# Kernel tuning notes

Measured on AMD Instinct MI355X. Metric: run time of the kernel, lower is better.

Reference implementation:

```python
import jax, jax.numpy as jnp
import numpy as np

B, BANDS, N, IN_C, F, C = 4096, 5, 30, 512, 128, 9

def setup_inputs() -> dict:
    key = jax.random.key(0)
    ks = jax.random.split(key, 10)
    def glorot(k, shape):
        lim = float(np.sqrt(6.0 / (shape[0] + shape[-1])))
        return jax.random.uniform(k, shape, jnp.float32, -lim, lim)
    return {
        "real": jax.random.normal(ks[0], (B, N, IN_C), jnp.float32),
        "imag": jax.random.normal(ks[1], (B, N, IN_C), jnp.float32),
        "graph": jax.random.normal(ks[2], (B, BANDS, N, N), jnp.float32),
        "W1": glorot(ks[3], (IN_C, F)),
        "b1": jnp.zeros((F,), jnp.float32),
        "W2": glorot(ks[4], (F, F)),
        "b2": jnp.zeros((F,), jnp.float32),
        "Wlin": glorot(ks[5], (F, 1)),
        "blin": jnp.zeros((1,), jnp.float32),
        "Wconv": glorot(ks[6], (C, N)),  # Conv1d(30, C, k=1) weight squeezed
        "bconv": jnp.zeros((C,), jnp.float32),
    }

def _norm_adj(graph):
    # adj = mean over bands; PyG from_scipy_sparse_matrix keeps only the
    # nonzero PATTERN (edge weights are discarded in the original code).
    adj = jnp.mean(graph, axis=1)                       # [B, N, N]
    A = (adj != 0).astype(jnp.float32)
    eye = jnp.eye(A.shape[-1], dtype=jnp.float32)
    A_hat = jnp.where(eye > 0, 1.0, A)                  # add remaining self-loops
    deg = A_hat.sum(-1)                                 # [B, N]
    dinv = jnp.where(deg > 0, jax.lax.rsqrt(deg), 0.0)
    return dinv[..., :, None] * A_hat * dinv[..., None, :]  # D^-1/2 (A+I) D^-1/2

def reference(real, imag, graph, W1, b1, W2, b2, Wlin, blin, Wconv, bconv):
    An = _norm_adj(graph)                               # [B, N, N]
    # GCNConv layer 1: propagate(x @ W) + bias, then ReLU (dropout = eval identity)
    h = jnp.einsum('bnm,bmf->bnf', An, real @ W1) + b1
    h = jax.nn.relu(h)
    # GCNConv layer 2
    h = jnp.einsum('bnm,bmf->bnf', An, h @ W2) + b2
    h = jax.nn.relu(h)
    # lin: [B, N, F] -> [B, N], relu, then Conv1d(30->C, k=1) over length-1 axis
    x = jax.nn.relu((h @ Wlin + blin).squeeze(-1))      # [B, N]
    out = x @ Wconv.T + bconv                           # [B, C]
    return out
```

## Files before the change

kernel.cpp:

```cpp
#include <hip/hip_runtime.h>
#include <cstdint>

#define B_SZ 4096
#define NN   30
#define INC  512
#define FF   128
#define CC   9

typedef short short8 __attribute__((ext_vector_type(8)));
typedef float f32x4 __attribute__((ext_vector_type(4)));
typedef unsigned short us4 __attribute__((ext_vector_type(4)));

__device__ inline void split_bf16(float x, unsigned short& hi, unsigned short& lo) {
  uint32_t bits = __float_as_uint(x);
  hi = (unsigned short)(bits >> 16);
  float hif = __uint_as_float(((uint32_t)hi) << 16);
  float r = x - hif;
  lo = (unsigned short)(__float_as_uint(r) >> 16);
}

__global__ __launch_bounds__(128) void k_norm_adj(const float* __restrict__ graph,
                                                  float* __restrict__ An) {
  __shared__ float Ah[NN * NN];
  __shared__ float dinv[NN];
  const int b = blockIdx.x;
  const float* g = graph + (long)b * 5 * NN * NN;
  for (int e = threadIdx.x; e < NN * NN; e += 128) {
    float s = g[e] + g[e + 900] + g[e + 1800] + g[e + 2700] + g[e + 3600];
    float mean = s * 0.2f;
    int i = e / NN;
    int j = e - i * NN;
    Ah[e] = (mean != 0.0f || i == j) ? 1.0f : 0.0f;
  }
  __syncthreads();
  if (threadIdx.x < NN) {
    float d = 0.f;
#pragma unroll
    for (int j = 0; j < NN; ++j) d += Ah[threadIdx.x * NN + j];
    dinv[threadIdx.x] = (d > 0.f) ? (1.0f / sqrtf(d)) : 0.0f;
  }
  __syncthreads();
  float* ob = An + (long)b * NN * NN;
  for (int e = threadIdx.x; e < NN * NN; e += 128) {
    int i = e / NN;
    int j = e - i * NN;
    ob[e] = Ah[e] * dinv[i] * dinv[j];
  }
}

__global__ __launch_bounds__(256) void k_prep_w(const float* __restrict__ W,
                                                unsigned short* __restrict__ Wth,
                                                unsigned short* __restrict__ Wtl,
                                                int K) {
  int idx = blockIdx.x * 256 + threadIdx.x;
  if (idx >= K * FF) return;
  int k = idx >> 7;
  int n = idx & 127;
  unsigned short h, l;
  split_bf16(W[idx], h, l);
  Wth[n * K + k] = h;
  Wtl[n * K + k] = l;
}

template <int K>
__global__ __launch_bounds__(256) void k_gemm_mfma(const float* __restrict__ A,
                                                   const unsigned short* __restrict__ Bth,
                                                   const unsigned short* __restrict__ Btl,
                                                   float* __restrict__ C) {
  constexpr int BK = 32;
  constexpr int LDT = 48;
  __shared__ unsigned short Ash[128 * LDT];
  __shared__ unsigned short Asl[128 * LDT];
  __shared__ unsigned short Bsh[128 * LDT];
  __shared__ unsigned short Bsl[128 * LDT];

  const int tid = threadIdx.x;
  const int wave = tid >> 6;
  const int lane = tid & 63;
  const int wrow = (wave >> 1) * 64;
  const int wcol = (wave & 1) * 64;
  const int fr = lane & 15;
  const int fq = lane >> 4;
  const long m0 = (long)blockIdx.x * 128;

  f32x4 acc[4][4];
#pragma unroll
  for (int i = 0; i < 4; ++i)
#pragma unroll
    for (int j = 0; j < 4; ++j) acc[i][j] = (f32x4){0.f, 0.f, 0.f, 0.f};

  for (int k0 = 0; k0 < K; k0 += BK) {
#pragma unroll
    for (int it = 0; it < 4; ++it) {
      int f = tid + it * 256;
      int row = f >> 3;
      int kq = f & 7;
      float4 v = *(const float4*)(A + (m0 + row) * (long)K + k0 + kq * 4);
      us4 h, l;
      split_bf16(v.x, ((unsigned short*)&h)[0], ((unsigned short*)&l)[0]);
      split_bf16(v.y, ((unsigned short*)&h)[1], ((unsigned short*)&l)[1]);
      split_bf16(v.z, ((unsigned short*)&h)[2], ((unsigned short*)&l)[2]);
      split_bf16(v.w, ((unsigned short*)&h)[3], ((unsigned short*)&l)[3]);
      *(us4*)(Ash + row * LDT + kq * 4) = h;
      *(us4*)(Asl + row * LDT + kq * 4) = l;
    }
#pragma unroll
    for (int it = 0; it < 4; ++it) {
      int f = tid + it * 256;
      int n = f >> 3;
      int kq = f & 7;
      us4 vh = *(const us4*)(Bth + (long)n * K + k0 + kq * 4);
      us4 vl = *(const us4*)(Btl + (long)n * K + k0 + kq * 4);
      *(us4*)(Bsh + n * LDT + kq * 4) = vh;
      *(us4*)(Bsl + n * LDT + kq * 4) = vl;
    }
    __syncthreads();

    short8 bh[4], bl[4];
#pragma unroll
    for (int ct = 0; ct < 4; ++ct) {
      int n = wcol + ct * 16 + fr;
      bh[ct] = *(const short8*)(Bsh + n * LDT + fq * 8);
      bl[ct] = *(const short8*)(Bsl + n * LDT + fq * 8);
    }
#pragma unroll
    for (int rt = 0; rt < 4; ++rt) {
      int m = wrow + rt * 16 + fr;
      short8 ah = *(const short8*)(Ash + m * LDT + fq * 8);
      short8 al = *(const short8*)(Asl + m * LDT + fq * 8);
#pragma unroll
      for (int ct = 0; ct < 4; ++ct) {
        acc[rt][ct] = __builtin_amdgcn_mfma_f32_16x16x32_bf16(ah, bh[ct], acc[rt][ct], 0, 0, 0);
        acc[rt][ct] = __builtin_amdgcn_mfma_f32_16x16x32_bf16(al, bh[ct], acc[rt][ct], 0, 0, 0);
        acc[rt][ct] = __builtin_amdgcn_mfma_f32_16x16x32_bf16(ah, bl[ct], acc[rt][ct], 0, 0, 0);
      }
    }
    __syncthreads();
  }

#pragma unroll
  for (int rt = 0; rt < 4; ++rt) {
#pragma unroll
    for (int ct = 0; ct < 4; ++ct) {
      int col = wcol + ct * 16 + fr;
#pragma unroll
      for (int r = 0; r < 4; ++r) {
        long row = m0 + wrow + rt * 16 + fq * 4 + r;
        C[row * FF + col] = acc[rt][ct][r];
      }
    }
  }
}

__global__ __launch_bounds__(128) void k_prop1(const float* __restrict__ An,
                                               const float* __restrict__ Y,
                                               const float* __restrict__ b1,
                                               float* __restrict__ H1) {
  const int b = blockIdx.x;
  const int f = threadIdx.x;
  const float* Yb = Y + (long)b * NN * FF + f;
  float y[NN];
#pragma unroll
  for (int m = 0; m < NN; ++m) y[m] = Yb[m * FF];
  const float* Ab = An + (long)b * NN * NN;
  const float bias = b1[f];
  float* Hb = H1 + (long)b * NN * FF + f;
#pragma unroll 1
  for (int i = 0; i < NN; ++i) {
    float acc = bias;
#pragma unroll
    for (int m = 0; m < NN; ++m) acc = fmaf(Ab[i * NN + m], y[m], acc);
    Hb[i * FF] = fmaxf(acc, 0.f);
  }
}

__global__ __launch_bounds__(128) void k_final(const float* __restrict__ An,
                                               const float* __restrict__ T,
                                               const float* __restrict__ b2,
                                               const float* __restrict__ Wlin,
                                               const float* __restrict__ blin,
                                               const float* __restrict__ Wconv,
                                               const float* __restrict__ bconv,
                                               float* __restrict__ out) {
  __shared__ float partial[2][NN];
  __shared__ float xs[NN];
  const int b = blockIdx.x;
  const int f = threadIdx.x;
  const int wave = f >> 6;
  const int lane = f & 63;
  const float* Tb = T + (long)b * NN * FF + f;
  float t[NN];
#pragma unroll
  for (int m = 0; m < NN; ++m) t[m] = Tb[m * FF];
  const float* Ab = An + (long)b * NN * NN;
  const float bias = b2[f];
  const float wl = Wlin[f];
#pragma unroll 1
  for (int i = 0; i < NN; ++i) {
    float acc = bias;
#pragma unroll
    for (int m = 0; m < NN; ++m) acc = fmaf(Ab[i * NN + m], t[m], acc);
    float c = fmaxf(acc, 0.f) * wl;
#pragma unroll
    for (int off = 32; off > 0; off >>= 1) c += __shfl_down(c, off, 64);
    if (lane == 0) partial[wave][i] = c;
  }
  __syncthreads();
  if (f < NN) {
    float x = partial[0][f] + partial[1][f] + blin[0];
    xs[f] = fmaxf(x, 0.f);
  }
  __syncthreads();
  if (f < CC) {
    float o = bconv[f];
#pragma unroll
    for (int i = 0; i < NN; ++i) o = fmaf(xs[i], Wconv[f * NN + i], o);
    out[(long)b * CC + f] = o;
  }
}

extern "C" void kernel_launch(void* const* d_in, const int* in_sizes, int n_in,
                              void* d_out, int out_size, void* d_ws, size_t ws_size,
                              hipStream_t stream) {
  const float* real  = (const float*)d_in[0];
  const float* graph = (const float*)d_in[2];
  const float* W1    = (const float*)d_in[3];
  const float* b1    = (const float*)d_in[4];
  const float* W2    = (const float*)d_in[5];
  const float* b2    = (const float*)d_in[6];
  const float* Wlin  = (const float*)d_in[7];
  const float* blin  = (const float*)d_in[8];
  const float* Wconv = (const float*)d_in[9];
  const float* bconv = (const float*)d_in[10];
  float* out = (float*)d_out;

  float* An = (float*)d_ws;
  float* Y  = An + (long)B_SZ * NN * NN;
  float* H1 = Y + (long)B_SZ * NN * FF;
  unsigned short* W1th = (unsigned short*)(H1 + (long)B_SZ * NN * FF);
  unsigned short* W1tl = W1th + INC * FF;
  unsigned short* W2th = W1tl + INC * FF;
  unsigned short* W2tl = W2th + FF * FF;
  float* T = Y;

  const int M = B_SZ * NN;

  k_norm_adj<<<B_SZ, 128, 0, stream>>>(graph, An);
  k_prep_w<<<(INC * FF + 255) / 256, 256, 0, stream>>>(W1, W1th, W1tl, INC);
  k_prep_w<<<(FF * FF + 255) / 256, 256, 0, stream>>>(W2, W2th, W2tl, FF);
  k_gemm_mfma<INC><<<M / 128, 256, 0, stream>>>(real, W1th, W1tl, Y);
  k_prop1<<<B_SZ, 128, 0, stream>>>(An, Y, b1, H1);
  k_gemm_mfma<FF><<<M / 128, 256, 0, stream>>>(H1, W2th, W2tl, T);
  k_final<<<B_SZ, 128, 0, stream>>>(An, T, b2, Wlin, blin, Wconv, bconv, out);
}
```

Baseline: 632.9 us.

## Fuse both GEMMs and propagations into one per-graph-pair kernel

Replaces the two MFMA GEMM kernels and the two propagation kernels with one kernel that processes two graphs per block (64 padded rows). Intermediate Y, H1 and T stay in LDS, with an XOR swizzle on H1 to avoid bank conflicts, so the large global round-trips of the intermediates are removed. The A tile is register-prefetched one K-step ahead, while W1/W2 fragments are read straight from global (L2). The trade-off is padding 60 rows to 64, the occupancy cap from about 64KB of LDS per block, and weight reloads from L2 in every block.

```diff
diff --git a/kernel.cpp b/kernel.cpp
--- a/kernel.cpp
+++ b/kernel.cpp
@@ -62,160 +62,216 @@
   Wtl[n * K + k] = l;
 }
 
-template <int K>
-__global__ __launch_bounds__(256) void k_gemm_mfma(const float* __restrict__ A,
-                                                   const unsigned short* __restrict__ Bth,
-                                                   const unsigned short* __restrict__ Btl,
-                                                   float* __restrict__ C) {
-  constexpr int BK = 32;
-  constexpr int LDT = 48;
-  __shared__ unsigned short Ash[128 * LDT];
-  __shared__ unsigned short Asl[128 * LDT];
-  __shared__ unsigned short Bsh[128 * LDT];
-  __shared__ unsigned short Bsl[128 * LDT];
+#define LDT 40
+#define LDY 132
+
+__global__ __launch_bounds__(256, 2) void k_fused(
+    const float* __restrict__ real,
+    const float* __restrict__ An,
+    const unsigned short* __restrict__ W1h, const unsigned short* __restrict__ W1l,
+    const unsigned short* __restrict__ W2h, const unsigned short* __restrict__ W2l,
+    const float* __restrict__ b1v, const float* __restrict__ b2v,
+    const float* __restrict__ Wlin, const float* __restrict__ blin,
+    const float* __restrict__ Wconv, const float* __restrict__ bconv,
+    float* __restrict__ out) {
+  __shared__ __align__(16) char smem[65168];
+  unsigned short* H1h = (unsigned short*)smem;
+  unsigned short* H1l = (unsigned short*)(smem + 16384);
+  unsigned short* Ash = (unsigned short*)(smem + 32768);
+  unsigned short* Asl = (unsigned short*)(smem + 32768 + 64 * LDT * 2);
+  float* Ylds = (float*)(smem + 32768);
+  float* partial = (float*)(smem + 64448);
+  float* xs = (float*)(smem + 64928);
 
   const int tid = threadIdx.x;
   const int wave = tid >> 6;
   const int lane = tid & 63;
-  const int wrow = (wave >> 1) * 64;
-  const int wcol = (wave & 1) * 64;
   const int fr = lane & 15;
   const int fq = lane >> 4;
-  const long m0 = (long)blockIdx.x * 128;
-
-  f32x4 acc[4][4];
+  const int wc = wave;
+  const long b0 = (long)blockIdx.x * 2;
+
+  f32x4 acc[4][2];
 #pragma unroll
   for (int i = 0; i < 4; ++i)
 #pragma unroll
-    for (int j = 0; j < 4; ++j) acc[i][j] = (f32x4){0.f, 0.f, 0.f, 0.f};
-
-  for (int k0 = 0; k0 < K; k0 += BK) {
-#pragma unroll
-    for (int it = 0; it < 4; ++it) {
-      int f = tid + it * 256;
-      int row = f >> 3;
-      int kq = f & 7;
-      float4 v = *(const float4*)(A + (m0 + row) * (long)K + k0 + kq * 4);
+    for (int j = 0; j < 2; ++j) acc[i][j] = (f32x4){0.f, 0.f, 0.f, 0.f};
+
+  const int r0 = tid >> 3, kq0 = tid & 7;
+  const int r1 = r0 + 32;
+  int i0 = r0 & 31; if (i0 >= NN) i0 -= NN;
+  int i1 = r1 & 31; if (i1 >= NN) i1 -= NN;
+  const float* aptr0 = real + ((b0 + (r0 >> 5)) * NN + i0) * (long)INC + kq0 * 4;
+  const float* aptr1 = real + ((b0 + (r1 >> 5)) * NN + i1) * (long)INC + kq0 * 4;
+
+  float4 pA0 = *(const float4*)(aptr0);
+  float4 pA1 = *(const float4*)(aptr1);
+
+  for (int k0 = 0; k0 < INC; k0 += 32) {
+    __syncthreads();
+    {
       us4 h, l;
-      split_bf16(v.x, ((unsigned short*)&h)[0], ((unsigned short*)&l)[0]);
-      split_bf16(v.y, ((unsigned short*)&h)[1], ((unsigned short*)&l)[1]);
-      split_bf16(v.z, ((unsigned short*)&h)[2], ((unsigned short*)&l)[2]);
-      split_bf16(v.w, ((unsigned short*)&h)[3], ((unsigned short*)&l)[3]);
-      *(us4*)(Ash + row * LDT + kq * 4) = h;
-      *(us4*)(Asl + row * LDT + kq * 4) = l;
-    }
-#pragma unroll
-    for (int it = 0; it < 4; ++it) {
-      int f = tid + it * 256;
-      int n = f >> 3;
-      int kq = f & 7;
-      us4 vh = *(const us4*)(Bth + (long)n * K + k0 + kq * 4);
-      us4 vl = *(const us4*)(Btl + (long)n * K + k0 + kq * 4);
-      *(us4*)(Bsh + n * LDT + kq * 4) = vh;
-      *(us4*)(Bsl + n * LDT + kq * 4) = vl;
+      split_bf16(pA0.x, ((unsigned short*)&h)[0], ((unsigned short*)&l)[0]);
+      split_bf16(pA0.y, ((unsigned short*)&h)[1], ((unsigned short*)&l)[1]);
+      split_bf16(pA0.z, ((unsigned short*)&h)[2], ((unsigned short*)&l)[2]);
+      split_bf16(pA0.w, ((unsigned short*)&h)[3], ((unsigned short*)&l)[3]);
+      *(us4*)(Ash + r0 * LDT + kq0 * 4) = h;
+      *(us4*)(Asl + r0 * LDT + kq0 * 4) = l;
+      split_bf16(pA1.x, ((unsigned short*)&h)[0], ((unsigned short*)&l)[0]);
+      split_bf16(pA1.y, ((unsigned short*)&h)[1], ((unsigned short*)&l)[1]);
+      split_bf16(pA1.z, ((unsigned short*)&h)[2], ((unsigned short*)&l)[2]);
+      split_bf16(pA1.w, ((unsigned short*)&h)[3], ((unsigned short*)&l)[3]);
+      *(us4*)(Ash + r1 * LDT + kq0 * 4) = h;
+      *(us4*)(Asl + r1 * LDT + kq0 * 4) = l;
+    }
+    if (k0 + 32 < INC) {
+      pA0 = *(const float4*)(aptr0 + k0 + 32);
+      pA1 = *(const float4*)(aptr1 + k0 + 32);
     }
     __syncthreads();
-
-    short8 bh[4], bl[4];
-#pragma unroll
-    for (int ct = 0; ct < 4; ++ct) {
-      int n = wcol + ct * 16 + fr;
-      bh[ct] = *(const short8*)(Bsh + n * LDT + fq * 8);
-      bl[ct] = *(const short8*)(Bsl + n * LDT + fq * 8);
+    short8 bh[2], bl2[2];
+#pragma unroll
+    for (int ct = 0; ct < 2; ++ct) {
+      const long n = wc * 32 + ct * 16 + fr;
+      bh[ct]  = *(const short8*)(W1h + n * INC + k0 + fq * 8);
+      bl2[ct] = *(const short8*)(W1l + n * INC + k0 + fq * 8);
     }
 #pragma unroll
     for (int rt = 0; rt < 4; ++rt) {
-      int m = wrow + rt * 16 + fr;
+      const int m = rt * 16 + fr;
       short8 ah = *(const short8*)(Ash + m * LDT + fq * 8);
       short8 al = *(const short8*)(Asl + m * LDT + fq * 8);
 #pragma unroll
-      for (int ct = 0; ct < 4; ++ct) {
+      for (int ct = 0; ct < 2; ++ct) {
         acc[rt][ct] = __builtin_amdgcn_mfma_f32_16x16x32_bf16(ah, bh[ct], acc[rt][ct], 0, 0, 0);
         acc[rt][ct] = __builtin_amdgcn_mfma_f32_16x16x32_bf16(al, bh[ct], acc[rt][ct], 0, 0, 0);
-        acc[rt][ct] = __builtin_amdgcn_mfma_f32_16x16x32_bf16(ah, bl[ct], acc[rt][ct], 0, 0, 0);
+        acc[rt][ct] = __builtin_amdgcn_mfma_f32_16x16x32_bf16(ah, bl2[ct], acc[rt][ct], 0, 0, 0);
       }
     }
-    __syncthreads();
-  }
+  }
+  __syncthreads();
 
 #pragma unroll
   for (int rt = 0; rt < 4; ++rt) {
 #pragma unroll
-    for (int ct = 0; ct < 4; ++ct) {
-      int col = wcol + ct * 16 + fr;
-#pragma unroll
-      for (int r = 0; r < 4; ++r) {
-        long row = m0 + wrow + rt * 16 + fq * 4 + r;
-        C[row * FF + col] = acc[rt][ct][r];
+    for (int r = 0; r < 4; ++r) {
+      const int row = rt * 16 + fq * 4 + r;
+      const int ii = row & 31;
+      if (ii < NN) {
+        const int yrow = (row >> 5) * NN + ii;
+#pragma unroll
+        for (int ct = 0; ct < 2; ++ct)
+          Ylds[yrow * LDY + wc * 32 + ct * 16 + fr] = acc[rt][ct][r];
       }
     }
   }
-}
-
-__global__ __launch_bounds__(128) void k_prop1(const float* __restrict__ An,
-                                               const float* __restrict__ Y,
-                                               const float* __restrict__ b1,
-                                               float* __restrict__ H1) {
-  const int b = blockIdx.x;
-  const int f = threadIdx.x;
-  const float* Yb = Y + (long)b * NN * FF + f;
-  float y[NN];
-#pragma unroll
-  for (int m = 0; m < NN; ++m) y[m] = Yb[m * FF];
-  const float* Ab = An + (long)b * NN * NN;
-  const float bias = b1[f];
-  float* Hb = H1 + (long)b * NN * FF + f;
+  {
+    const int pr = wave;
+    const int prow = (pr >> 1) * 32 + 30 + (pr & 1);
+    *(uint32_t*)(H1h + prow * 128 + lane * 2) = 0u;
+    *(uint32_t*)(H1l + prow * 128 + lane * 2) = 0u;
+  }
+  __syncthreads();
+
+  const int f = tid & 127;
+  const int bu = __builtin_amdgcn_readfirstlane(tid >> 7);
+  const float* Arow = An + (b0 + bu) * (NN * NN);
+  {
+    float y[NN];
+#pragma unroll
+    for (int m = 0; m < NN; ++m) y[m] = Ylds[(bu * NN + m) * LDY + f];
+    const float bias1 = b1v[f];
 #pragma unroll 1
-  for (int i = 0; i < NN; ++i) {
-    float acc = bias;
-#pragma unroll
-    for (int m = 0; m < NN; ++m) acc = fmaf(Ab[i * NN + m], y[m], acc);
-    Hb[i * FF] = fmaxf(acc, 0.f);
-  }
-}
-
-__global__ __launch_bounds__(128) void k_final(const float* __restrict__ An,
-                                               const float* __restrict__ T,
-                                               const float* __restrict__ b2,
-                                               const float* __restrict__ Wlin,
-                                               const float* __restrict__ blin,
-                                               const float* __restrict__ Wconv,
-                                               const float* __restrict__ bconv,
-                                               float* __restrict__ out) {
-  __shared__ float partial[2][NN];
-  __shared__ float xs[NN];
-  const int b = blockIdx.x;
-  const int f = threadIdx.x;
-  const int wave = f >> 6;
-  const int lane = f & 63;
-  const float* Tb = T + (long)b * NN * FF + f;
-  float t[NN];
-#pragma unroll
-  for (int m = 0; m < NN; ++m) t[m] = Tb[m * FF];
-  const float* Ab = An + (long)b * NN * NN;
-  const float bias = b2[f];
-  const float wl = Wlin[f];
+    for (int i = 0; i < NN; ++i) {
+      float h = bias1;
+#pragma unroll
+      for (int m = 0; m < NN; ++m) h = fmaf(Arow[i * NN + m], y[m], h);
+      h = fmaxf(h, 0.f);
+      unsigned short hh, hl;
+      split_bf16(h, hh, hl);
+      const int row = bu * 32 + i;
+      const int idx = row * 128 + ((((f >> 3) ^ (row & 7)) << 3) | (f & 7));
+      H1h[idx] = hh;
+      H1l[idx] = hl;
+    }
+  }
+  __syncthreads();
+
+  f32x4 acc2[4][2];
+#pragma unroll
+  for (int i = 0; i < 4; ++i)
+#pragma unroll
+    for (int j = 0; j < 2; ++j) acc2[i][j] = (f32x4){0.f, 0.f, 0.f, 0.f};
+
+#pragma unroll
+  for (int ks = 0; ks < 4; ++ks) {
+    short8 bh[2], bl2[2];
+#pragma unroll
+    for (int ct = 0; ct < 2; ++ct) {
+      const long n = wc * 32 + ct * 16 + fr;
+      bh[ct]  = *(const short8*)(W2h + n * FF + ks * 32 + fq * 8);
+      bl2[ct] = *(const short8*)(W2l + n * FF + ks * 32 + fq * 8);
+    }
+#pragma unroll
+    for (int rt = 0; rt < 4; ++rt) {
+      const int row = rt * 16 + fr;
+      const int gs = (((ks * 4 + fq) ^ (row & 7)) << 3);
+      short8 ah = *(const short8*)(H1h + row * 128 + gs);
+      short8 al = *(const short8*)(H1l + row * 128 + gs);
+#pragma unroll
+      for (int ct = 0; ct < 2; ++ct) {
+        acc2[rt][ct] = __builtin_amdgcn_mfma_f32_16x16x32_bf16(ah, bh[ct], acc2[rt][ct], 0, 0, 0);
+        acc2[rt][ct] = __builtin_amdgcn_mfma_f32_16x16x32_bf16(al, bh[ct], acc2[rt][ct], 0, 0, 0);
+        acc2[rt][ct] = __builtin_amdgcn_mfma_f32_16x16x32_bf16(ah, bl2[ct], acc2[rt][ct], 0, 0, 0);
+      }
+    }
+  }
+#pragma unroll
+  for (int rt = 0; rt < 4; ++rt) {
+#pragma unroll
+    for (int r = 0; r < 4; ++r) {
+      const int row = rt * 16 + fq * 4 + r;
+      const int ii = row & 31;
+      if (ii < NN) {
+        const int yrow = (row >> 5) * NN + ii;
+#pragma unroll
+        for (int ct = 0; ct < 2; ++ct)
+          Ylds[yrow * LDY + wc * 32 + ct * 16 + fr] = acc2[rt][ct][r];
+      }
+    }
+  }
+  __syncthreads();
+
+  {
+    float t[NN];
+#pragma unroll
+    for (int m = 0; m < NN; ++m) t[m] = Ylds[(bu * NN + m) * LDY + f];
+    const float bias2 = b2v[f];
+    const float wl = Wlin[f];
 #pragma unroll 1
-  for (int i = 0; i < NN; ++i) {
-    float acc = bias;
-#pragma unroll
-    for (int m = 0; m < NN; ++m) acc = fmaf(Ab[i * NN + m], t[m], acc);
-    float c = fmaxf(acc, 0.f) * wl;
-#pragma unroll
-    for (int off = 32; off > 0; off >>= 1) c += __shfl_down(c, off, 64);
-    if (lane == 0) partial[wave][i] = c;
-  }
-  __syncthreads();
-  if (f < NN) {
-    float x = partial[0][f] + partial[1][f] + blin[0];
-    xs[f] = fmaxf(x, 0.f);
-  }
-  __syncthreads();
-  if (f < CC) {
-    float o = bconv[f];
-#pragma unroll
-    for (int i = 0; i < NN; ++i) o = fmaf(xs[i], Wconv[f * NN + i], o);
-    out[(long)b * CC + f] = o;
+    for (int i = 0; i < NN; ++i) {
+      float h = bias2;
+#pragma unroll
+      for (int m = 0; m < NN; ++m) h = fmaf(Arow[i * NN + m], t[m], h);
+      float c = fmaxf(h, 0.f) * wl;
+#pragma unroll
+      for (int off = 32; off > 0; off >>= 1) c += __shfl_down(c, off, 64);
+      if (lane == 0) partial[wave * NN + i] = c;
+    }
+  }
+  __syncthreads();
+  if (tid < 2 * NN) {
+    const int bb = tid / NN, i = tid - bb * NN;
+    float x = partial[bb * 2 * NN + i] + partial[(bb * 2 + 1) * NN + i] + blin[0];
+    xs[bb * NN + i] = fmaxf(x, 0.f);
+  }
+  __syncthreads();
+  if (tid < 2 * CC) {
+    const int bb = tid / CC, c = tid - bb * CC;
+    float o = bconv[c];
+#pragma unroll
+    for (int i = 0; i < NN; ++i) o = fmaf(xs[bb * NN + i], Wconv[c * NN + i], o);
+    out[(b0 + bb) * CC + c] = o;
   }
 }
 
@@ -235,21 +291,14 @@
   float* out = (float*)d_out;
 
   float* An = (float*)d_ws;
-  float* Y  = An + (long)B_SZ * NN * NN;
-  float* H1 = Y + (long)B_SZ * NN * FF;
-  unsigned short* W1th = (unsigned short*)(H1 + (long)B_SZ * NN * FF);
-  unsigned short* W1tl = W1th + INC * FF;
-  unsigned short* W2th = W1tl + INC * FF;
-  unsigned short* W2tl = W2th + FF * FF;
-  float* T = Y;
-
-  const int M = B_SZ * NN;
+  unsigned short* W1h = (unsigned short*)(An + (long)B_SZ * NN * NN);
+  unsigned short* W1l = W1h + INC * FF;
+  unsigned short* W2h = W1l + INC * FF;
+  unsigned short* W2l = W2h + FF * FF;
 
   k_norm_adj<<<B_SZ, 128, 0, stream>>>(graph, An);
-  k_prep_w<<<(INC * FF + 255) / 256, 256, 0, stream>>>(W1, W1th, W1tl, INC);
-  k_prep_w<<<(FF * FF + 255) / 256, 256, 0, stream>>>(W2, W2th, W2tl, FF);
-  k_gemm_mfma<INC><<<M / 128, 256, 0, stream>>>(real, W1th, W1tl, Y);
-  k_prop1<<<B_SZ, 128, 0, stream>>>(An, Y, b1, H1);
-  k_gemm_mfma<FF><<<M / 128, 256, 0, stream>>>(H1, W2th, W2tl, T);
-  k_final<<<B_SZ, 128, 0, stream>>>(An, T, b2, Wlin, blin, Wconv, bconv, out);
-}
+  k_prep_w<<<(INC * FF + 255) / 256, 256, 0, stream>>>(W1, W1h, W1l, INC);
+  k_prep_w<<<(FF * FF + 255) / 256, 256, 0, stream>>>(W2, W2h, W2l, FF);
+  k_fused<<<B_SZ / 2, 256, 0, stream>>>(real, An, W1h, W1l, W2h, W2l,
+                                        b1, b2, Wlin, blin, Wconv, bconv, out);
+}
```

After: 651.7 us. 1.03x slower.
